# Kernel tuning notes

Hardware: AMD Instinct MI355X
Metric: run time of the kernel (lower is better)

## Reference

```python
import jax, jax.numpy as jnp
import numpy as np

BLOCK_SIZE = 32
FP6_E2M3_MAX = 7.5

def _build_fp6_e2m3_grid():
    vals = set()
    for bits in range(64):
        s = (bits >> 5) & 1
        e = (bits >> 3) & 3
        m = bits & 7
        v = (m / 8.0) if e == 0 else (1.0 + m / 8.0) * 2.0 ** (e - 1)
        vals.add(-v if s else v)
    return np.array(sorted(vals), dtype=np.float32)

_GRID = jnp.asarray(_build_fp6_e2m3_grid())  # sorted 1-D fp32 grid (46 unique values)

def _nearest_on_grid(x, grid):
    # round-to-nearest on a sorted grid via searchsorted (matches torch reference)
    idx = jnp.clip(jnp.searchsorted(grid, x), 0, grid.shape[0] - 1)
    idx_lo = jnp.maximum(idx - 1, 0)
    v_hi = grid[idx]
    v_lo = grid[idx_lo]
    return jnp.where(jnp.abs(x - v_lo) <= jnp.abs(x - v_hi), v_lo, v_hi)

def _mx_quantize(t, eps=1e-30):
    # t: (rows, K) fp32, K divisible by BLOCK_SIZE
    rows, K = t.shape
    blocks = t.reshape(rows, K // BLOCK_SIZE, BLOCK_SIZE)
    scales = jnp.maximum(jnp.max(jnp.abs(blocks), axis=-1) / FP6_E2M3_MAX, eps)  # (rows, nb)
    q = _nearest_on_grid(blocks / scales[..., None], _GRID)  # fp6-simulated fp32
    return q, scales

def setup_inputs() -> dict:
    key = jax.random.key(0)
    k1, k2, k3 = jax.random.split(key, 3)
    x = jax.random.normal(k1, (8, 8192, 1024), dtype=jnp.float32)
    weight = jax.random.normal(k2, (1024, 1024), dtype=jnp.float32) * 0.02
    bias = jax.random.normal(k3, (1024,), dtype=jnp.float32) * 0.02
    return {"x": x, "weight": weight, "bias": bias}

def reference(x, weight, bias):
    batch_shape = x.shape[:-1]
    in_features = x.shape[-1]
    x2 = x.astype(jnp.float32).reshape(-1, in_features)      # (N, K)
    w2 = weight.astype(jnp.float32)                           # (J, K)
    xq, xs = _mx_quantize(x2)                                 # (N, nb, bs), (N, nb)
    wq, ws = _mx_quantize(w2)                                 # (J, nb, bs), (J, nb)
    # out[n, j] = sum_b xs[n,b] * ws[j,b] * dot(xq[n,b,:], wq[j,b,:])
    # == dequant(x) @ dequant(w).T  (fold fp32 scales into quantized blocks)
    xd = (xq * xs[..., None]).reshape(x2.shape)
    wd = (wq * ws[..., None]).reshape(w2.shape)
    out = xd @ wd.T + bias
    return out.reshape(*batch_shape, -1)
```

## Files before the change

### kernel.cpp

```cpp
#include <hip/hip_runtime.h>
#include <stdint.h>

#define K_DIM 1024
#define N_DIM 1024
#define M_DIM 65536

typedef __bf16 bf16_t;
typedef __bf16 bf16x8 __attribute__((ext_vector_type(8)));
typedef float f32x4 __attribute__((ext_vector_type(4)));

#define GLOAD_LDS16(g, l) __builtin_amdgcn_global_load_lds( \
    (const __attribute__((address_space(1))) void*)(g),     \
    (__attribute__((address_space(3))) void*)(l), 16, 0, 0)

#define VMCNT(n) asm volatile("s_waitcnt vmcnt(%0)" ::"n"(n) : "memory")
#define LGKM(n) asm volatile("s_waitcnt lgkmcnt(%0)" ::"n"(n) : "memory")
#define SCHEDB() __builtin_amdgcn_sched_barrier(0)

__global__ __launch_bounds__(256) void quant_dequant_kernel(
    const float* __restrict__ x, bf16_t* __restrict__ xd, long long nx,
    const float* __restrict__ w, bf16_t* __restrict__ wd, long long nw) {
  const float* in;
  bf16_t* out;
  long long i, stride, n;
  if (blockIdx.x < 512) {
    in = w; out = wd; n = nw;
    i = (long long)blockIdx.x * blockDim.x + threadIdx.x;
    stride = 512ll * blockDim.x;
  } else {
    in = x; out = xd; n = nx;
    i = (long long)(blockIdx.x - 512) * blockDim.x + threadIdx.x;
    stride = (long long)(gridDim.x - 512) * blockDim.x;
  }
  for (; i < n; i += stride) {
    long long base = i * 8;
    f32x4 v0 = *reinterpret_cast<const f32x4*>(in + base);
    f32x4 v1 = *reinterpret_cast<const f32x4*>(in + base + 4);
    float mx = 0.0f;
#pragma unroll
    for (int j = 0; j < 4; ++j) {
      mx = fmaxf(mx, fabsf(v0[j]));
      mx = fmaxf(mx, fabsf(v1[j]));
    }
    mx = fmaxf(mx, __shfl_xor(mx, 1));
    mx = fmaxf(mx, __shfl_xor(mx, 2));
    float s = fmaxf(mx / 7.5f, 1e-30f);
    bf16x8 o;
#pragma unroll
    for (int j = 0; j < 8; ++j) {
      float xv = (j < 4) ? v0[j] : v1[j - 4];
      float y = xv / s;
      float m = fabsf(y);
      float h, hinv;
      if (m < 2.0f)      { h = 0.125f; hinv = 8.0f; }
      else if (m < 4.0f) { h = 0.25f;  hinv = 4.0f; }
      else               { h = 0.5f;   hinv = 2.0f; }
      float nn = m * hinv;
      float kf = floorf(nn);
      float fr = nn - kf;
      float up = (fr > 0.5f || (fr == 0.5f && y < 0.0f)) ? 1.0f : 0.0f;
      float q = fminf((kf + up) * h, 7.5f);
      o[j] = (bf16_t)(copysignf(q, y) * s);
    }
    *reinterpret_cast<bf16x8*>(out + base) = o;
  }
}

__global__ __launch_bounds__(512, 2) void mx_gemm(
    const bf16_t* __restrict__ A, const bf16_t* __restrict__ B,
    const float* __restrict__ bias, float* __restrict__ C) {
  __shared__ char lds[131072];

  const int tid = threadIdx.x;
  const int lane = tid & 63;
  const int wid = tid >> 6;
  const int wm = wid >> 2;
  const int wn = wid & 3;

  const int b = blockIdx.x;
  const int xcd = b & 7;
  const int t = b >> 3;
  const int m_tile = xcd * 32 + (t >> 2);
  const int n_tile = t & 3;

  const int R0 = tid >> 2;
  const int c0 = ((tid & 3) ^ ((tid >> 3) & 3)) * 8;
  const bf16_t* aS0 = A + (size_t)(m_tile * 256 + R0) * K_DIM + c0;
  const bf16_t* aS1 = aS0 + (size_t)128 * K_DIM;
  const bf16_t* bS0 = B + (size_t)(n_tile * 256 + R0) * K_DIM + c0;
  const bf16_t* bS1 = bS0 + (size_t)128 * K_DIM;
  const int dst16 = tid * 16;

#define STG_A(KOFF, SLOT)                           \
  {                                                 \
    char* d_ = lds + (SLOT) * 16384 + dst16;        \
    GLOAD_LDS16(aS0 + (KOFF), d_);                  \
    GLOAD_LDS16(aS1 + (KOFF), d_ + 8192);           \
  }
#define STG_B(KOFF, SLOT)                           \
  {                                                 \
    char* d_ = lds + (SLOT) * 16384 + dst16;        \
    GLOAD_LDS16(bS0 + (KOFF), d_);                  \
    GLOAD_LDS16(bS1 + (KOFF), d_ + 8192);           \
  }

  const int swz = (((lane >> 4) ^ ((lane >> 1) & 3)) << 4);
  const int aRd = (wm * 128 + (lane & 15)) * 64 + swz;
  const int bRd = (wn * 64 + (lane & 15)) * 64 + swz;

  f32x4 acc[8][4];
#pragma unroll
  for (int i = 0; i < 8; ++i)
#pragma unroll
    for (int j = 0; j < 4; ++j) acc[i][j] = (f32x4)(0.0f);

#define SLICE(SQ, KOFF, DO_STG, DO_V, VN)                                    \
  {                                                                          \
    const char* cA_ = lds + (((2 * (SQ)) & 7) * 16384);                      \
    const char* cB_ = lds + (((2 * (SQ) + 1) & 7) * 16384);                  \
    bf16x8 af[4], bf[4];                                                     \
                                                           \
    _Pragma("unroll") for (int i = 0; i < 4; ++i) af[i] =                    \
        *reinterpret_cast<const bf16x8*>(cA_ + aRd + i * 1024);              \
    _Pragma("unroll") for (int j = 0; j < 4; ++j) bf[j] =                    \
        *reinterpret_cast<const bf16x8*>(cB_ + bRd + j * 1024);              \
    if (DO_STG) {                                                            \
      STG_A((KOFF) + 64, ((2 * (SQ) + 4) & 7));                              \
      STG_B((KOFF) + 64, ((2 * (SQ) + 5) & 7));                              \
    }                                                                        \
    SCHEDB();                                                                \
    __builtin_amdgcn_s_barrier();                                            \
    LGKM(0);                                                                 \
    SCHEDB();                                                                \
    __builtin_amdgcn_s_setprio(1);                                           \
    _Pragma("unroll") for (int i = 0; i < 4; ++i)                            \
        _Pragma("unroll") for (int j = 0; j < 4; ++j) acc[i][j] =            \
            __builtin_amdgcn_mfma_f32_16x16x32_bf16(af[i], bf[j],            \
                                                    acc[i][j], 0, 0, 0);     \
    __builtin_amdgcn_s_setprio(0);                                           \
    SCHEDB();                                                                \
    __builtin_amdgcn_s_barrier();                                            \
                                                           \
    _Pragma("unroll") for (int i = 0; i < 4; ++i) af[i] =                    \
        *reinterpret_cast<const bf16x8*>(cA_ + aRd + 4096 + i * 1024);       \
    if (DO_V) { VMCNT(VN); }                                                 \
    SCHEDB();                                                                \
    __builtin_amdgcn_s_barrier();                                            \
    LGKM(0);                                                                 \
    SCHEDB();                                                                \
    __builtin_amdgcn_s_setprio(1);                                           \
    _Pragma("unroll") for (int i = 0; i < 4; ++i)                            \
        _Pragma("unroll") for (int j = 0; j < 4; ++j) acc[4 + i][j] =        \
            __builtin_amdgcn_mfma_f32_16x16x32_bf16(af[i], bf[j],            \
                                                    acc[4 + i][j], 0, 0, 0); \
    __builtin_amdgcn_s_setprio(0);                                           \
    SCHEDB();                                                                \
    __builtin_amdgcn_s_barrier();                                            \
  }

  STG_A(0, 0);
  STG_B(0, 1);
  STG_A(32, 2);
  STG_B(32, 3);
  VMCNT(4);
  __builtin_amdgcn_s_barrier();

  for (int g = 0; g < 7; ++g) {
    SLICE(0, 0, 1, 1, 4);
    SLICE(1, 32, 1, 1, 4);
    SLICE(2, 64, 1, 1, 4);
    SLICE(3, 96, 1, 1, 4);
    aS0 += 128;
    aS1 += 128;
    bS0 += 128;
    bS1 += 128;
  }
  SLICE(0, 0, 1, 1, 4);
  SLICE(1, 32, 1, 1, 4);
  SLICE(2, 64, 0, 1, 0);
  SLICE(3, 96, 0, 0, 0);

  const int col0 = n_tile * 256 + wn * 64 + (lane & 15);
  const int row0 = m_tile * 256 + wm * 128 + ((lane >> 4) << 2);
#pragma unroll
  for (int j = 0; j < 4; ++j) {
    float bv = bias[col0 + j * 16];
#pragma unroll
    for (int m = 0; m < 8; ++m) {
#pragma unroll
      for (int r = 0; r < 4; ++r) {
        C[(size_t)(row0 + m * 16 + r) * N_DIM + col0 + j * 16] =
            acc[m][j][r] + bv;
      }
    }
  }
#undef STG_A
#undef STG_B
#undef SLICE
}

extern "C" void kernel_launch(void* const* d_in, const int* in_sizes, int n_in,
                              void* d_out, int out_size, void* d_ws,
                              size_t ws_size, hipStream_t stream) {
  const float* x = (const float*)d_in[0];
  const float* w = (const float*)d_in[1];
  const float* bias = (const float*)d_in[2];
  float* out = (float*)d_out;

  bf16_t* xd = (bf16_t*)d_ws;
  bf16_t* wd = xd + (size_t)M_DIM * K_DIM;

  quant_dequant_kernel<<<4608, 256, 0, stream>>>(
      x, xd, (long long)M_DIM * K_DIM / 8, w, wd,
      (long long)K_DIM * N_DIM / 8);

  mx_gemm<<<(M_DIM / 256) * (N_DIM / 256), 512, 0, stream>>>(xd, wd, bias,
                                                             out);
}
```

Before: 271.6 us.

## Shrink GEMM tile to 256x128 and load B fragments straight from global

The GEMM block tile changes from 256x256 with 8 waves to 256x128 with 4 waves, and LDS is halved to 64KB. Only A is now staged through LDS, in a 4-slot ring. Each wave loads its B fragments directly from global memory into registers, double-buffered, so the B LDS round trip and the second barrier per slice go away. The cost is uncoalesced global reads for B (16-byte strided per lane) and less reuse of B across waves, which relies on the cache to hold the small weight matrix.

Measured after the change: 338.5 us. +24.6%, slower.

```diff
diff --git a/kernel.cpp b/kernel.cpp
--- a/kernel.cpp
+++ b/kernel.cpp
@@ -66,47 +66,40 @@
   }
 }
 
-__global__ __launch_bounds__(512, 2) void mx_gemm(
+__global__ __launch_bounds__(256, 2) void mx_gemm(
     const bf16_t* __restrict__ A, const bf16_t* __restrict__ B,
     const float* __restrict__ bias, float* __restrict__ C) {
-  __shared__ char lds[131072];
+  __shared__ char lds[65536];
 
   const int tid = threadIdx.x;
   const int lane = tid & 63;
   const int wid = tid >> 6;
-  const int wm = wid >> 2;
-  const int wn = wid & 3;
+  const int wm = wid >> 1;
+  const int wn = wid & 1;
 
   const int b = blockIdx.x;
   const int xcd = b & 7;
   const int t = b >> 3;
-  const int m_tile = xcd * 32 + (t >> 2);
-  const int n_tile = t & 3;
+  const int m_tile = xcd * 32 + (t >> 3);
+  const int n_tile = t & 7;
 
   const int R0 = tid >> 2;
   const int c0 = ((tid & 3) ^ ((tid >> 3) & 3)) * 8;
-  const bf16_t* aS0 = A + (size_t)(m_tile * 256 + R0) * K_DIM + c0;
-  const bf16_t* aS1 = aS0 + (size_t)128 * K_DIM;
-  const bf16_t* bS0 = B + (size_t)(n_tile * 256 + R0) * K_DIM + c0;
-  const bf16_t* bS1 = bS0 + (size_t)128 * K_DIM;
+  const bf16_t* aSg[4];
+#pragma unroll
+  for (int g = 0; g < 4; ++g)
+    aSg[g] = A + (size_t)(m_tile * 256 + g * 64 + R0) * K_DIM + c0;
   const int dst16 = tid * 16;
-
-#define STG_A(KOFF, SLOT)                           \
-  {                                                 \
-    char* d_ = lds + (SLOT) * 16384 + dst16;        \
-    GLOAD_LDS16(aS0 + (KOFF), d_);                  \
-    GLOAD_LDS16(aS1 + (KOFF), d_ + 8192);           \
-  }
-#define STG_B(KOFF, SLOT)                           \
-  {                                                 \
-    char* d_ = lds + (SLOT) * 16384 + dst16;        \
-    GLOAD_LDS16(bS0 + (KOFF), d_);                  \
-    GLOAD_LDS16(bS1 + (KOFF), d_ + 8192);           \
-  }
 
   const int swz = (((lane >> 4) ^ ((lane >> 1) & 3)) << 4);
   const int aRd = (wm * 128 + (lane & 15)) * 64 + swz;
-  const int bRd = (wn * 64 + (lane & 15)) * 64 + swz;
+
+  const char* Bb = (const char*)B;
+  int boff[4];
+#pragma unroll
+  for (int j = 0; j < 4; ++j)
+    boff[j] = (n_tile * 128 + wn * 64 + j * 16 + (lane & 15)) * 2048 +
+              (lane >> 4) * 16;
 
   f32x4 acc[8][4];
 #pragma unroll
@@ -114,73 +107,65 @@
 #pragma unroll
     for (int j = 0; j < 4; ++j) acc[i][j] = (f32x4)(0.0f);
 
-#define SLICE(SQ, KOFF, DO_STG, DO_V, VN)                                    \
+  bf16x8 bfr[2][4];
+
+#define SLICE(Q, VTOP, VB, DO_B, DO_STG)                                     \
   {                                                                          \
-    const char* cA_ = lds + (((2 * (SQ)) & 7) * 16384);                      \
-    const char* cB_ = lds + (((2 * (SQ) + 1) & 7) * 16384);                  \
-    bf16x8 af[4], bf[4];                                                     \
-                                                           \
-    _Pragma("unroll") for (int i = 0; i < 4; ++i) af[i] =                    \
-        *reinterpret_cast<const bf16x8*>(cA_ + aRd + i * 1024);              \
-    _Pragma("unroll") for (int j = 0; j < 4; ++j) bf[j] =                    \
-        *reinterpret_cast<const bf16x8*>(cB_ + bRd + j * 1024);              \
+    VMCNT(VTOP);                                                             \
+    __builtin_amdgcn_s_barrier();                                            \
+    SCHEDB();                                                                \
+    const char* sb_ = lds + ((Q) & 3) * 16384;                               \
+    bf16x8 af[8];                                                            \
+    _Pragma("unroll") for (int i = 0; i < 8; ++i) af[i] =                    \
+        *reinterpret_cast<const bf16x8*>(sb_ + aRd + i * 1024);              \
+    if (DO_B) {                                                              \
+      _Pragma("unroll") for (int j = 0; j < 4; ++j)                          \
+          bfr[((Q) + 1) & 1][j] = *reinterpret_cast<const bf16x8*>(          \
+              Bb + boff[j] + ((Q) + 1) * 64);                                \
+    }                                                                        \
     if (DO_STG) {                                                            \
-      STG_A((KOFF) + 64, ((2 * (SQ) + 4) & 7));                              \
-      STG_B((KOFF) + 64, ((2 * (SQ) + 5) & 7));                              \
+      _Pragma("unroll") for (int g = 0; g < 4; ++g)                          \
+          GLOAD_LDS16(aSg[g] + ((Q) + 2) * 32,                               \
+                      lds + (((Q) + 2) & 3) * 16384 + g * 4096 + dst16);     \
     }                                                                        \
     SCHEDB();                                                                \
-    __builtin_amdgcn_s_barrier();                                            \
+    VMCNT(VB);                                                               \
     LGKM(0);                                                                 \
     SCHEDB();                                                                \
     __builtin_amdgcn_s_setprio(1);                                           \
-    _Pragma("unroll") for (int i = 0; i < 4; ++i)                            \
+    _Pragma("unroll") for (int i = 0; i < 8; ++i)                            \
         _Pragma("unroll") for (int j = 0; j < 4; ++j) acc[i][j] =            \
-            __builtin_amdgcn_mfma_f32_16x16x32_bf16(af[i], bf[j],            \
+            __builtin_amdgcn_mfma_f32_16x16x32_bf16(af[i], bfr[(Q) & 1][j],  \
                                                     acc[i][j], 0, 0, 0);     \
     __builtin_amdgcn_s_setprio(0);                                           \
-    SCHEDB();                                                                \
-    __builtin_amdgcn_s_barrier();                                            \
-                                                           \
-    _Pragma("unroll") for (int i = 0; i < 4; ++i) af[i] =                    \
-        *reinterpret_cast<const bf16x8*>(cA_ + aRd + 4096 + i * 1024);       \
-    if (DO_V) { VMCNT(VN); }                                                 \
-    SCHEDB();                                                                \
-    __builtin_amdgcn_s_barrier();                                            \
-    LGKM(0);                                                                 \
-    SCHEDB();                                                                \
-    __builtin_amdgcn_s_setprio(1);                                           \
-    _Pragma("unroll") for (int i = 0; i < 4; ++i)                            \
-        _Pragma("unroll") for (int j = 0; j < 4; ++j) acc[4 + i][j] =        \
-            __builtin_amdgcn_mfma_f32_16x16x32_bf16(af[i], bf[j],            \
-                                                    acc[4 + i][j], 0, 0, 0); \
-    __builtin_amdgcn_s_setprio(0);                                           \
-    SCHEDB();                                                                \
-    __builtin_amdgcn_s_barrier();                                            \
-  }
-
-  STG_A(0, 0);
-  STG_B(0, 1);
-  STG_A(32, 2);
-  STG_B(32, 3);
-  VMCNT(4);
-  __builtin_amdgcn_s_barrier();
-
-  for (int g = 0; g < 7; ++g) {
-    SLICE(0, 0, 1, 1, 4);
-    SLICE(1, 32, 1, 1, 4);
-    SLICE(2, 64, 1, 1, 4);
-    SLICE(3, 96, 1, 1, 4);
-    aS0 += 128;
-    aS1 += 128;
-    bS0 += 128;
-    bS1 += 128;
-  }
-  SLICE(0, 0, 1, 1, 4);
-  SLICE(1, 32, 1, 1, 4);
-  SLICE(2, 64, 0, 1, 0);
-  SLICE(3, 96, 0, 0, 0);
-
-  const int col0 = n_tile * 256 + wn * 64 + (lane & 15);
+  }
+
+#pragma unroll
+  for (int g = 0; g < 4; ++g)
+    GLOAD_LDS16(aSg[g], lds + g * 4096 + dst16);
+#pragma unroll
+  for (int j = 0; j < 4; ++j)
+    bfr[0][j] = *reinterpret_cast<const bf16x8*>(Bb + boff[j]);
+#pragma unroll
+  for (int g = 0; g < 4; ++g)
+    GLOAD_LDS16(aSg[g] + 32, lds + 16384 + g * 4096 + dst16);
+
+  for (int grp = 0; grp < 7; ++grp) {
+    SLICE(0, 8, 12, 1, 1);
+    SLICE(1, 8, 12, 1, 1);
+    SLICE(2, 8, 12, 1, 1);
+    SLICE(3, 8, 12, 1, 1);
+#pragma unroll
+    for (int g = 0; g < 4; ++g) aSg[g] += 128;
+#pragma unroll
+    for (int j = 0; j < 4; ++j) boff[j] += 256;
+  }
+  SLICE(0, 8, 12, 1, 1);
+  SLICE(1, 8, 12, 1, 1);
+  SLICE(2, 8, 8, 1, 0);
+  SLICE(3, 4, 0, 0, 0);
+
+  const int col0 = n_tile * 128 + wn * 64 + (lane & 15);
   const int row0 = m_tile * 256 + wm * 128 + ((lane >> 4) << 2);
 #pragma unroll
   for (int j = 0; j < 4; ++j) {
@@ -194,8 +179,6 @@
       }
     }
   }
-#undef STG_A
-#undef STG_B
 #undef SLICE
 }
 
@@ -214,6 +197,6 @@
       x, xd, (long long)M_DIM * K_DIM / 8, w, wd,
       (long long)K_DIM * N_DIM / 8);
 
-  mx_gemm<<<(M_DIM / 256) * (N_DIM / 256), 512, 0, stream>>>(xd, wd, bias,
+  mx_gemm<<<(M_DIM / 256) * (N_DIM / 128), 256, 0, stream>>>(xd, wd, bias,
                                                              out);
 }
```
